# Kernel optimization log

Measured on AMD Instinct MI355X. Metric: run time of the kernel, lower is better.

The kernel has to match this reference:

```python
import jax, jax.numpy as jnp
import numpy as np

D_MODEL = 512
NUM_HEADS = 8
D_K = D_MODEL // NUM_HEADS


def setup_inputs() -> dict:
    key = jax.random.key(0)
    ks = jax.random.split(key, 24)
    inp = {
        "user": jax.random.normal(ks[0], (4, 8192, D_MODEL), jnp.float32),
        "mood": jax.random.normal(ks[1], (3, 8192, D_MODEL), jnp.float32),
        "genre": jax.random.normal(ks[2], (5, 8192, D_MODEL), jnp.float32),
    }
    i = 3
    for p in ["l", "s", "zl", "zs"]:
        inp[p + "_w1"] = jax.random.normal(ks[i], (D_K, D_K), jnp.float32) * 0.1; i += 1
        inp[p + "_b1"] = jax.random.normal(ks[i], (D_K,), jnp.float32) * 0.1; i += 1
        inp[p + "_w2"] = jax.random.normal(ks[i], (D_K,), jnp.float32) * 0.1; i += 1
        inp[p + "_b2"] = jax.random.normal(ks[i], (1,), jnp.float32) * 0.1; i += 1
    inp["lin_w"] = jax.random.normal(ks[i], (D_MODEL, D_MODEL), jnp.float32) * 0.05; i += 1
    inp["lin_b"] = jax.random.normal(ks[i], (D_MODEL,), jnp.float32) * 0.05
    return inp


def _score(x, w1, b1, w2, b2):
    # Linear(d_k,d_k) -> Sigmoid -> Linear(d_k,1); returns [..., 1]
    h = jax.nn.sigmoid(jnp.einsum("...k,jk->...j", x, w1) + b1)
    return (jnp.einsum("...k,k->...", h, w2) + b2)[..., None]


def reference(user, mood, genre,
              l_w1, l_b1, l_w2, l_b2,
              s_w1, s_b1, s_w2, s_b2,
              zl_w1, zl_b1, zl_w2, zl_b2,
              zs_w1, zs_b1, zs_w2, zs_b2,
              lin_w, lin_b):
    scale = 1.0 / np.sqrt(D_K).astype(np.float32)
    Nu, B, D = user.shape
    Nm = mood.shape[0]
    Ng = genre.shape[0]
    # L[u,g] = split_heads(user_u * genre_g) / sqrt(d_k)  -> [Nu, Ng, B, H, d_k]
    L = (user[:, None] * genre[None, :]).reshape(Nu, Ng, B, NUM_HEADS, D_K) * scale
    S = (mood[:, None] * genre[None, :]).reshape(Nm, Ng, B, NUM_HEADS, D_K) * scale
    L_score = _score(L, l_w1, l_b1, l_w2, l_b2)  # [Nu, Ng, B, H, 1]
    S_score = _score(S, s_w1, s_b1, s_w2, s_b2)
    # sum over all key pairs of score * value -> [B, H, d_k]
    L_att = jnp.sum(L_score * L, axis=(0, 1))
    S_att = jnp.sum(S_score * S, axis=(0, 1))
    rl = _score(L_att, zl_w1, zl_b1, zl_w2, zl_b2)  # [B, H, 1]
    rs = _score(S_att, zs_w1, zs_b1, zs_w2, zs_b2)
    r = jax.nn.softmax(jnp.concatenate([rl, rs], axis=-1), axis=-1)
    out = r[..., 0:1] * L_att + r[..., 1:2] * S_att  # [B, H, d_k]
    out = out.reshape(B, NUM_HEADS * D_K)
    return out @ lin_w.T + lin_b
```

## Files before the change

kernel.cpp:

```cpp
#include <hip/hip_runtime.h>
#include <hip/hip_bf16.h>
#include <stdint.h>

#define B_TOK 8192
#define DMODEL 512

typedef __attribute__((ext_vector_type(4))) float f32x4;
typedef __attribute__((ext_vector_type(8))) short bf16x8;
typedef __attribute__((ext_vector_type(4))) short bf16x4;
typedef __attribute__((ext_vector_type(2))) _Float16 f16x2;
typedef __attribute__((ext_vector_type(4))) _Float16 f16x4;
typedef __attribute__((ext_vector_type(8))) _Float16 f16x8;

__device__ __forceinline__ short f2bf(float f) {
    union { float f; uint32_t u; } v; v.f = f;
    uint32_t r = (v.u + 0x7fffu + ((v.u >> 16) & 1u)) >> 16;
    return (short)r;
}

__device__ __forceinline__ f16x2 pkrtz(float a, float b) {
    auto r = __builtin_amdgcn_cvt_pkrtz(a, b);
    union { decltype(r) i; f16x2 o; } u; u.i = r;
    return u.o;
}

__device__ __forceinline__ float sigm2(float x) {
    return __builtin_amdgcn_rcpf(1.0f + __builtin_amdgcn_exp2f(x));
}

#define NL2E (-1.44269504089f)
#define L2E  (1.44269504089f)

struct ScoreW {
    f16x8 w1f[4][2];
    f32x4 b1f[4];
    f16x8 w2f[2];
    f32x4 b2v;
};

template <bool EXPS>
__device__ __forceinline__ void load_scorew(ScoreW& W,
    const float* __restrict__ w1p, const float* __restrict__ b1p,
    const float* __restrict__ w2p, const float* __restrict__ b2p,
    int tl, int g16)
{
    const float scl = EXPS ? NL2E : 1.0f;
    #pragma unroll
    for (int nt = 0; nt < 4; ++nt) {
        const int q  = nt >> 1;
        const int hi = (nt & 1) * 4;
        const int j  = q * 32 + (tl >> 2) * 8 + hi + (tl & 3);
        #pragma unroll
        for (int kk = 0; kk < 2; ++kk) {
            const float* wr = w1p + j * 64 + kk * 32 + g16 * 8;
            f32x4 a0 = *(const f32x4*)wr * scl;
            f32x4 a1 = *(const f32x4*)(wr + 4) * scl;
            f16x2 p0 = pkrtz(a0[0], a0[1]);
            f16x2 p1 = pkrtz(a0[2], a0[3]);
            f16x2 p2 = pkrtz(a1[0], a1[1]);
            f16x2 p3 = pkrtz(a1[2], a1[3]);
            f16x8 f = {p0[0],p0[1],p1[0],p1[1],p2[0],p2[1],p3[0],p3[1]};
            W.w1f[nt][kk] = f;
        }
        W.b1f[nt] = *(const f32x4*)(b1p + q * 32 + g16 * 8 + hi) * scl;
    }
    #pragma unroll
    for (int q = 0; q < 2; ++q) {
        const float* wp = w2p + q * 32 + g16 * 8;
        f32x4 a0 = *(const f32x4*)wp;
        f32x4 a1 = *(const f32x4*)(wp + 4);
        f16x2 p0 = pkrtz(a0[0], a0[1]);
        f16x2 p1 = pkrtz(a0[2], a0[3]);
        f16x2 p2 = pkrtz(a1[0], a1[1]);
        f16x2 p3 = pkrtz(a1[2], a1[3]);
        f16x8 f = {p0[0],p0[1],p1[0],p1[1],p2[0],p2[1],p3[0],p3[1]};
        W.w2f[q] = f;
    }
    const float b2 = b2p[0];
    f32x4 bb = {b2, b2, b2, b2};
    W.b2v = bb;
}

template <bool POLY>
__device__ __forceinline__ f32x4 score16(const ScoreW& W, f16x8 xa0, f16x8 xa1)
{
    f32x4 acc1[4];
    #pragma unroll
    for (int nt = 0; nt < 4; ++nt)
        acc1[nt] = __builtin_amdgcn_mfma_f32_16x16x32_f16(W.w1f[nt][0], xa0, W.b1f[nt], 0, 0, 0);
    #pragma unroll
    for (int nt = 0; nt < 4; ++nt)
        acc1[nt] = __builtin_amdgcn_mfma_f32_16x16x32_f16(W.w1f[nt][1], xa1, acc1[nt], 0, 0, 0);

    f32x4 acc2a = W.b2v;
    f32x4 acc2b = {0.f, 0.f, 0.f, 0.f};
    #pragma unroll
    for (int q = 0; q < 2; ++q) {
        f16x8 sb;
        if constexpr (POLY) {
            const _Float16 c1 = (_Float16)0.25f;
            const _Float16 c2 = (_Float16)(-0.0208333f);
            const _Float16 c3 = (_Float16)(0.00208333f);
            const _Float16 hf = (_Float16)0.5f;
            f16x2 h0 = pkrtz(acc1[2*q][0],   acc1[2*q][1]);
            f16x2 h1 = pkrtz(acc1[2*q][2],   acc1[2*q][3]);
            f16x2 h2 = pkrtz(acc1[2*q+1][0], acc1[2*q+1][1]);
            f16x2 h3 = pkrtz(acc1[2*q+1][2], acc1[2*q+1][3]);
            f16x8 hv = {h0[0],h0[1],h1[0],h1[1],h2[0],h2[1],h3[0],h3[1]};
            f16x8 C1 = {c1,c1,c1,c1,c1,c1,c1,c1};
            f16x8 C2 = {c2,c2,c2,c2,c2,c2,c2,c2};
            f16x8 C3 = {c3,c3,c3,c3,c3,c3,c3,c3};
            f16x8 HF = {hf,hf,hf,hf,hf,hf,hf,hf};
            f16x8 hh = hv * hv;
            f16x8 u  = hh * C3 + C2;
            f16x8 v  = hh * u  + C1;
            sb       = hv * v  + HF;
        } else {
            f16x2 s0 = pkrtz(sigm2(acc1[2*q][0]),   sigm2(acc1[2*q][1]));
            f16x2 s1 = pkrtz(sigm2(acc1[2*q][2]),   sigm2(acc1[2*q][3]));
            f16x2 s2 = pkrtz(sigm2(acc1[2*q+1][0]), sigm2(acc1[2*q+1][1]));
            f16x2 s3 = pkrtz(sigm2(acc1[2*q+1][2]), sigm2(acc1[2*q+1][3]));
            sb = (f16x8){s0[0],s0[1],s1[0],s1[1],s2[0],s2[1],s3[0],s3[1]};
        }
        if (q == 0)
            acc2a = __builtin_amdgcn_mfma_f32_16x16x32_f16(W.w2f[0], sb, acc2a, 0, 0, 0);
        else
            acc2b = __builtin_amdgcn_mfma_f32_16x16x32_f16(W.w2f[1], sb, acc2b, 0, 0, 0);
    }
    return acc2a + acc2b;
}

template <bool WSB>
__global__ __launch_bounds__(256, 3) void fused_att(
    const float* __restrict__ user, const float* __restrict__ mood,
    const float* __restrict__ genre,
    const float* __restrict__ lw1,  const float* __restrict__ lb1,
    const float* __restrict__ lw2,  const float* __restrict__ lb2,
    const float* __restrict__ sw1,  const float* __restrict__ sb1,
    const float* __restrict__ sw2,  const float* __restrict__ sb2,
    const float* __restrict__ zlw1, const float* __restrict__ zlb1,
    const float* __restrict__ zlw2, const float* __restrict__ zlb2,
    const float* __restrict__ zsw1, const float* __restrict__ zsb1,
    const float* __restrict__ zsw2, const float* __restrict__ zsb2,
    float* __restrict__ fout, short* __restrict__ bout)
{
    __shared__ __attribute__((aligned(16))) unsigned char smraw[12 * 32 * 128];
    _Float16* att = (_Float16*)smraw;
    float*    rsc = (float*)(smraw + 20480);

    const int tid  = threadIdx.x;
    const int lane = tid & 63;
    const int wv   = tid >> 6;
    const int tl   = lane & 15;
    const int g16  = lane >> 4;
    const int wg   = blockIdx.x;

    {
        const int k4 = (tid & 15) << 2;
        #pragma unroll
        for (int h = 0; h < 2; ++h) {
            const int r = h * 16 + (tid >> 4);
            const int dst_off = r * 128 + ((k4 * 2) ^ ((r & 7) << 4));
            const size_t src_off = (size_t)wg * 2048 + (size_t)r * 64 + k4;
            #pragma unroll
            for (int a = 0; a < 12; ++a) {
                const float* src; float scl;
                if (a < 4)      { src = user  + (size_t)a       * (B_TOK * DMODEL); scl = 0.125f; }
                else if (a < 9) { src = genre + (size_t)(a - 4) * (B_TOK * DMODEL); scl = 1.0f;  }
                else            { src = mood  + (size_t)(a - 9) * (B_TOK * DMODEL); scl = 0.125f; }
                f32x4 v = *(const f32x4*)(src + src_off) * scl;
                f16x2 lo = pkrtz(v[0], v[1]);
                f16x2 hi = pkrtz(v[2], v[3]);
                f16x4 b = {lo[0], lo[1], hi[0], hi[1]};
                *(f16x4*)(smraw + a * 4096 + dst_off) = b;
            }
        }
    }
    __syncthreads();

    ScoreW W;
    if (wv < 2) load_scorew<false>(W, lw1, lb1, lw2, lb2, tl, g16);
    else        load_scorew<false>(W, sw1, sb1, sw2, sb2, tl, g16);

    int pcount, sbase, pstart;
    if      (wv == 0) { pstart = 0;  pcount = 10; sbase = 0; }
    else if (wv == 1) { pstart = 10; pcount = 10; sbase = 0; }
    else if (wv == 2) { pstart = 0;  pcount = 8;  sbase = 9; }
    else              { pstart = 8;  pcount = 7;  sbase = 9; }

    int aA = sbase + pstart / 5;
    int aB = 4 + pstart % 5;

    f16x8 attA0 = {0,0,0,0,0,0,0,0}, attA1 = {0,0,0,0,0,0,0,0};
    f16x8 attB0 = {0,0,0,0,0,0,0,0}, attB1 = {0,0,0,0,0,0,0,0};

    const unsigned char* lbase = smraw;
    const int rowbA = tl * 128;
    const int rowbB = (16 + tl) * 128;
    const int swz   = (tl & 7) << 4;
    const int ko2   = g16 * 16;
    const int o0 = ko2 ^ swz;
    const int o1 = (ko2 + 64) ^ swz;

    for (int pi = 0; pi < pcount; ++pi) {
        const unsigned char* ub = lbase + aA * 4096;
        const unsigned char* gb = lbase + aB * 4096;
        f16x8 xaA0 = *(const f16x8*)(ub + rowbA + o0) * *(const f16x8*)(gb + rowbA + o0);
        f16x8 xaA1 = *(const f16x8*)(ub + rowbA + o1) * *(const f16x8*)(gb + rowbA + o1);
        f16x8 xaB0 = *(const f16x8*)(ub + rowbB + o0) * *(const f16x8*)(gb + rowbB + o0);
        f16x8 xaB1 = *(const f16x8*)(ub + rowbB + o1) * *(const f16x8*)(gb + rowbB + o1);

        f32x4 scA = score16<true>(W, xaA0, xaA1);
        f32x4 scB = score16<true>(W, xaB0, xaB1);

        _Float16 hA = (_Float16)scA[0];
        _Float16 hB = (_Float16)scB[0];
        f16x8 svA = {hA, hA, hA, hA, hA, hA, hA, hA};
        f16x8 svB = {hB, hB, hB, hB, hB, hB, hB, hB};
        attA0 += svA * xaA0;
        attA1 += svA * xaA1;
        attB0 += svB * xaB0;
        attB1 += svB * xaB1;

        if (++aB == 9) { aB = 4; ++aA; }
    }

    __syncthreads();

    *(f16x8*)(att + (wv * 32 + tl) * 80 + g16 * 8)           = attA0;
    *(f16x8*)(att + (wv * 32 + tl) * 80 + 32 + g16 * 8)      = attA1;
    *(f16x8*)(att + (wv * 32 + 16 + tl) * 80 + g16 * 8)      = attB0;
    *(f16x8*)(att + (wv * 32 + 16 + tl) * 80 + 32 + g16 * 8) = attB1;
    __syncthreads();

    if (wv < 2) {
        ScoreW ZW;
        if (wv == 0) load_scorew<true>(ZW, zlw1, zlb1, zlw2, zlb2, tl, g16);
        else         load_scorew<true>(ZW, zsw1, zsb1, zsw2, zsb2, tl, g16);

        const int b0 = wv * 2, b1i = wv * 2 + 1;
        #pragma unroll
        for (int g = 0; g < 2; ++g) {
            const int r = g * 16 + tl;
            f16x8 za0 = *(const f16x8*)(att + (b0  * 32 + r) * 80 + g16 * 8) +
                        *(const f16x8*)(att + (b1i * 32 + r) * 80 + g16 * 8);
            f16x8 za1 = *(const f16x8*)(att + (b0  * 32 + r) * 80 + 32 + g16 * 8) +
                        *(const f16x8*)(att + (b1i * 32 + r) * 80 + 32 + g16 * 8);
            f32x4 rz = score16<false>(ZW, za0, za1);
            if (g16 == 0) rsc[wv * 32 + r] = rz[0];
        }
    }
    __syncthreads();

    {
        const int k4 = (tid & 15) << 2;
        #pragma unroll
        for (int h = 0; h < 2; ++h) {
            const int r = h * 16 + (tid >> 4);
            f16x4 Lh = *(const f16x4*)(att + (0 * 32 + r) * 80 + k4) +
                       *(const f16x4*)(att + (1 * 32 + r) * 80 + k4);
            f16x4 Sh = *(const f16x4*)(att + (2 * 32 + r) * 80 + k4) +
                       *(const f16x4*)(att + (3 * 32 + r) * 80 + k4);
            const float rl = rsc[r], rs = rsc[32 + r];
            const float r0 = __builtin_amdgcn_rcpf(1.0f + __builtin_amdgcn_exp2f((rs - rl) * L2E));
            float o[4];
            #pragma unroll
            for (int i = 0; i < 4; ++i) {
                const float Lf = (float)Lh[i], Sf = (float)Sh[i];
                o[i] = Sf + (Lf - Sf) * r0;
            }
            const size_t base = (size_t)wg * 2048 + (size_t)r * 64 + k4;
            if constexpr (WSB) {
                bf16x4 b = {f2bf(o[0]), f2bf(o[1]), f2bf(o[2]), f2bf(o[3])};
                *(bf16x4*)(bout + base) = b;
            } else {
                f32x4 mx = {o[0], o[1], o[2], o[3]};
                *(f32x4*)(fout + base) = mx;
            }
        }
    }
}

__global__ __launch_bounds__(256) void conv_w(const float* __restrict__ w,
                                              short* __restrict__ o)
{
    const size_t i = ((size_t)blockIdx.x * 256 + threadIdx.x) * 4;
    f32x4 v = *(const f32x4*)(w + i);
    bf16x4 b;
    b[0] = f2bf(v[0]); b[1] = f2bf(v[1]); b[2] = f2bf(v[2]); b[3] = f2bf(v[3]);
    *(bf16x4*)(o + i) = b;
}

__global__ __launch_bounds__(256, 2) void final_gemm_ws(
    const short* __restrict__ A, const short* __restrict__ Bw,
    const float* __restrict__ bias, float* __restrict__ C)
{
    __shared__ __attribute__((aligned(16))) short lA[64 * 64];
    __shared__ __attribute__((aligned(16))) short lB[128 * 64];

    const int tid  = threadIdx.x;
    const int lane = tid & 63;
    const int wv   = tid >> 6;
    const int tl   = lane & 15;
    const int g16  = lane >> 4;
    const int wr   = wv >> 1;
    const int wc   = wv & 1;
    const int bm   = blockIdx.x & 127;
    const int bn   = blockIdx.x >> 7;
    const int m0   = bm * 64, n0 = bn * 128;

    f32x4 acc[2][4];
    #pragma unroll
    for (int mt = 0; mt < 2; ++mt)
        #pragma unroll
        for (int nt = 0; nt < 4; ++nt) { f32x4 z = {0.f,0.f,0.f,0.f}; acc[mt][nt] = z; }

    bf16x8 ra[2], rb[4];
    auto LD = [&](int ks) {
        #pragma unroll
        for (int i = 0; i < 2; ++i) {
            const int c = tid + i * 256;
            ra[i] = *(const bf16x8*)(A + (size_t)(m0 + (c >> 3)) * 512 + ks * 64 + (c & 7) * 8);
        }
        #pragma unroll
        for (int i = 0; i < 4; ++i) {
            const int c = tid + i * 256;
            rb[i] = *(const bf16x8*)(Bw + (size_t)(n0 + (c >> 3)) * 512 + ks * 64 + (c & 7) * 8);
        }
    };

    LD(0);
    for (int ks = 0; ks < 8; ++ks) {
        __syncthreads();
        #pragma unroll
        for (int i = 0; i < 2; ++i) {
            const int c = tid + i * 256, row = c >> 3;
            *(bf16x8*)(lA + row * 64 + ((c & 7) ^ (row & 7)) * 8) = ra[i];
        }
        #pragma unroll
        for (int i = 0; i < 4; ++i) {
            const int c = tid + i * 256, row = c >> 3;
            *(bf16x8*)(lB + row * 64 + ((c & 7) ^ (row & 7)) * 8) = rb[i];
        }
        __syncthreads();
        if (ks < 7) LD(ks + 1);
        #pragma unroll
        for (int kk = 0; kk < 2; ++kk) {
            bf16x8 af[2], bfr[4];
            #pragma unroll
            for (int mt = 0; mt < 2; ++mt) {
                const int row = wr * 32 + mt * 16 + tl;
                af[mt] = *(const bf16x8*)(lA + row * 64 + ((kk * 4 + g16) ^ (row & 7)) * 8);
            }
            #pragma unroll
            for (int nt = 0; nt < 4; ++nt) {
                const int row = wc * 64 + nt * 16 + tl;
                bfr[nt] = *(const bf16x8*)(lB + row * 64 + ((kk * 4 + g16) ^ (row & 7)) * 8);
            }
            #pragma unroll
            for (int mt = 0; mt < 2; ++mt)
                #pragma unroll
                for (int nt = 0; nt < 4; ++nt)
                    acc[mt][nt] = __builtin_amdgcn_mfma_f32_16x16x32_bf16(af[mt], bfr[nt], acc[mt][nt], 0, 0, 0);
        }
    }

    #pragma unroll
    for (int nt = 0; nt < 4; ++nt) {
        const int n = n0 + wc * 64 + nt * 16 + tl;
        const float bv = bias[n];
        #pragma unroll
        for (int mt = 0; mt < 2; ++mt) {
            #pragma unroll
            for (int r = 0; r < 4; ++r) {
                C[(size_t)(m0 + wr * 32 + mt * 16 + g16 * 4 + r) * 512 + n] = acc[mt][nt][r] + bv;
            }
        }
    }
}

__global__ __launch_bounds__(256, 2) void final_gemm_ip(
    const float* __restrict__ linw, const float* __restrict__ linb, float* io)
{
    const int tid  = threadIdx.x;
    const int lane = tid & 63;
    const int wv   = tid >> 6;
    const int tl   = lane & 15;
    const int g16  = lane >> 4;
    const int row0 = blockIdx.x * 64 + wv * 16;

    f32x4 acc[32];
    #pragma unroll
    for (int nt = 0; nt < 32; ++nt) { f32x4 z = {0.f,0.f,0.f,0.f}; acc[nt] = z; }

    for (int ks = 0; ks < 16; ++ks) {
        const int k0 = ks * 32 + g16 * 8;
        const float* ar = io + (size_t)(row0 + tl) * 512 + k0;
        f32x4 a0 = *(const f32x4*)ar;
        f32x4 a1 = *(const f32x4*)(ar + 4);
        bf16x8 af;
        af[0]=f2bf(a0[0]); af[1]=f2bf(a0[1]); af[2]=f2bf(a0[2]); af[3]=f2bf(a0[3]);
        af[4]=f2bf(a1[0]); af[5]=f2bf(a1[1]); af[6]=f2bf(a1[2]); af[7]=f2bf(a1[3]);
        #pragma unroll
        for (int nt = 0; nt < 32; ++nt) {
            const int n = nt * 16 + tl;
            const float* br = linw + (size_t)n * 512 + k0;
            f32x4 b0 = *(const f32x4*)br;
            f32x4 b1 = *(const f32x4*)(br + 4);
            bf16x8 bv;
            bv[0]=f2bf(b0[0]); bv[1]=f2bf(b0[1]); bv[2]=f2bf(b0[2]); bv[3]=f2bf(b0[3]);
            bv[4]=f2bf(b1[0]); bv[5]=f2bf(b1[1]); bv[6]=f2bf(b1[2]); bv[7]=f2bf(b1[3]);
            acc[nt] = __builtin_amdgcn_mfma_f32_16x16x32_bf16(af, bv, acc[nt], 0, 0, 0);
        }
    }

    #pragma unroll
    for (int nt = 0; nt < 32; ++nt) {
        const int n = nt * 16 + tl;
        const float lb = linb[n];
        #pragma unroll
        for (int r = 0; r < 4; ++r)
            io[(size_t)(row0 + g16 * 4 + r) * 512 + n] = acc[nt][r] + lb;
    }
}

extern "C" void kernel_launch(void* const* d_in, const int* in_sizes, int n_in,
                              void* d_out, int out_size, void* d_ws, size_t ws_size,
                              hipStream_t stream)
{
    const float* user = (const float*)d_in[0];
    const float* mood = (const float*)d_in[1];
    const float* genre= (const float*)d_in[2];
    const float* lw1  = (const float*)d_in[3];
    const float* lb1  = (const float*)d_in[4];
    const float* lw2  = (const float*)d_in[5];
    const float* lb2  = (const float*)d_in[6];
    const float* sw1  = (const float*)d_in[7];
    const float* sb1  = (const float*)d_in[8];
    const float* sw2  = (const float*)d_in[9];
    const float* sb2  = (const float*)d_in[10];
    const float* zlw1 = (const float*)d_in[11];
    const float* zlb1 = (const float*)d_in[12];
    const float* zlw2 = (const float*)d_in[13];
    const float* zlb2 = (const float*)d_in[14];
    const float* zsw1 = (const float*)d_in[15];
    const float* zsb1 = (const float*)d_in[16];
    const float* zsw2 = (const float*)d_in[17];
    const float* zsb2 = (const float*)d_in[18];
    const float* linw = (const float*)d_in[19];
    const float* linb = (const float*)d_in[20];
    float* out = (float*)d_out;

    const size_t WNEED = (size_t)512 * 512 * 2 + (size_t)B_TOK * 512 * 2;
    if (ws_size >= WNEED) {
        short* wb   = (short*)d_ws;
        short* mixb = wb + 512 * 512;
        conv_w<<<256, 256, 0, stream>>>(linw, wb);
        fused_att<true><<<B_TOK / 4, 256, 0, stream>>>(
            user, mood, genre,
            lw1, lb1, lw2, lb2, sw1, sb1, sw2, sb2,
            zlw1, zlb1, zlw2, zlb2, zsw1, zsb1, zsw2, zsb2,
            nullptr, mixb);
        final_gemm_ws<<<512, 256, 0, stream>>>(mixb, wb, linb, out);
    } else {
        fused_att<false><<<B_TOK / 4, 256, 0, stream>>>(
            user, mood, genre,
            lw1, lb1, lw2, lb2, sw1, sb1, sw2, sb2,
            zlw1, zlb1, zlw2, zlb2, zsw1, zsb1, zsw2, zsb2,
            out, nullptr);
        final_gemm_ip<<<B_TOK / 64, 256, 0, stream>>>(linw, linb, out);
    }
}
```

Measured before the change: 75.82 us.

## Load inputs directly into registers and split attention work by row instead of pair

```diff
diff --git a/kernel.cpp b/kernel.cpp
--- a/kernel.cpp
+++ b/kernel.cpp
@@ -31,6 +31,16 @@
 #define NL2E (-1.44269504089f)
 #define L2E  (1.44269504089f)
 
+__device__ __forceinline__ f16x8 ldh(const float* __restrict__ p, float scl) {
+    f32x4 a0 = *(const f32x4*)p * scl;
+    f32x4 a1 = *(const f32x4*)(p + 4) * scl;
+    f16x2 p0 = pkrtz(a0[0], a0[1]);
+    f16x2 p1 = pkrtz(a0[2], a0[3]);
+    f16x2 p2 = pkrtz(a1[0], a1[1]);
+    f16x2 p3 = pkrtz(a1[2], a1[3]);
+    return (f16x8){p0[0],p0[1],p1[0],p1[1],p2[0],p2[1],p3[0],p3[1]};
+}
+
 struct ScoreW {
     f16x8 w1f[4][2];
     f32x4 b1f[4];
@@ -51,31 +61,13 @@
         const int hi = (nt & 1) * 4;
         const int j  = q * 32 + (tl >> 2) * 8 + hi + (tl & 3);
         #pragma unroll
-        for (int kk = 0; kk < 2; ++kk) {
-            const float* wr = w1p + j * 64 + kk * 32 + g16 * 8;
-            f32x4 a0 = *(const f32x4*)wr * scl;
-            f32x4 a1 = *(const f32x4*)(wr + 4) * scl;
-            f16x2 p0 = pkrtz(a0[0], a0[1]);
-            f16x2 p1 = pkrtz(a0[2], a0[3]);
-            f16x2 p2 = pkrtz(a1[0], a1[1]);
-            f16x2 p3 = pkrtz(a1[2], a1[3]);
-            f16x8 f = {p0[0],p0[1],p1[0],p1[1],p2[0],p2[1],p3[0],p3[1]};
-            W.w1f[nt][kk] = f;
-        }
+        for (int kk = 0; kk < 2; ++kk)
+            W.w1f[nt][kk] = ldh(w1p + j * 64 + kk * 32 + g16 * 8, scl);
         W.b1f[nt] = *(const f32x4*)(b1p + q * 32 + g16 * 8 + hi) * scl;
     }
     #pragma unroll
-    for (int q = 0; q < 2; ++q) {
-        const float* wp = w2p + q * 32 + g16 * 8;
-        f32x4 a0 = *(const f32x4*)wp;
-        f32x4 a1 = *(const f32x4*)(wp + 4);
-        f16x2 p0 = pkrtz(a0[0], a0[1]);
-        f16x2 p1 = pkrtz(a0[2], a0[3]);
-        f16x2 p2 = pkrtz(a1[0], a1[1]);
-        f16x2 p3 = pkrtz(a1[2], a1[3]);
-        f16x8 f = {p0[0],p0[1],p1[0],p1[1],p2[0],p2[1],p3[0],p3[1]};
-        W.w2f[q] = f;
-    }
+    for (int q = 0; q < 2; ++q)
+        W.w2f[q] = ldh(w2p + q * 32 + g16 * 8, 1.0f);
     const float b2 = b2p[0];
     f32x4 bb = {b2, b2, b2, b2};
     W.b2v = bb;
@@ -131,7 +123,7 @@
 }
 
 template <bool WSB>
-__global__ __launch_bounds__(256, 3) void fused_att(
+__global__ __launch_bounds__(256, 2) void fused_att(
     const float* __restrict__ user, const float* __restrict__ mood,
     const float* __restrict__ genre,
     const float* __restrict__ lw1,  const float* __restrict__ lb1,
@@ -144,9 +136,9 @@
     const float* __restrict__ zsw2, const float* __restrict__ zsb2,
     float* __restrict__ fout, short* __restrict__ bout)
 {
-    __shared__ __attribute__((aligned(16))) unsigned char smraw[12 * 32 * 128];
-    _Float16* att = (_Float16*)smraw;
-    float*    rsc = (float*)(smraw + 20480);
+    __shared__ __attribute__((aligned(16))) _Float16 attL[32][80];
+    __shared__ __attribute__((aligned(16))) _Float16 attS[32][80];
+    __shared__ float rls[2][32];
 
     const int tid  = threadIdx.x;
     const int lane = tid & 63;
@@ -155,128 +147,106 @@
     const int g16  = lane >> 4;
     const int wg   = blockIdx.x;
 
+    const int  rbase  = (wv & 1) * 16;
+    const bool isL    = (wv < 2);
+    const size_t rowoff = ((size_t)wg * 32 + rbase + tl) * 64 + g16 * 8;
+
+    ScoreW W;
+    if (isL) load_scorew<false>(W, lw1, lb1, lw2, lb2, tl, g16);
+    else     load_scorew<false>(W, sw1, sb1, sw2, sb2, tl, g16);
+
+    f16x8 att0 = {0,0,0,0,0,0,0,0};
+    f16x8 att1 = {0,0,0,0,0,0,0,0};
+
+    if (isL) {
+        f16x8 uf[4][2], gf[5][2];
+        #pragma unroll
+        for (int a = 0; a < 4; ++a) {
+            const float* p = user + (size_t)a * (B_TOK * DMODEL) + rowoff;
+            uf[a][0] = ldh(p, 0.125f);
+            uf[a][1] = ldh(p + 32, 0.125f);
+        }
+        #pragma unroll
+        for (int a = 0; a < 5; ++a) {
+            const float* p = genre + (size_t)a * (B_TOK * DMODEL) + rowoff;
+            gf[a][0] = ldh(p, 1.0f);
+            gf[a][1] = ldh(p + 32, 1.0f);
+        }
+        #pragma unroll
+        for (int pi = 0; pi < 20; ++pi) {
+            const int aA = pi / 5, aB = pi % 5;
+            f16x8 xa0 = uf[aA][0] * gf[aB][0];
+            f16x8 xa1 = uf[aA][1] * gf[aB][1];
+            f32x4 sc = score16<true>(W, xa0, xa1);
+            _Float16 hs = (_Float16)sc[0];
+            f16x8 sv = {hs,hs,hs,hs,hs,hs,hs,hs};
+            att0 += sv * xa0;
+            att1 += sv * xa1;
+        }
+    } else {
+        f16x8 mf[3][2], gf[5][2];
+        #pragma unroll
+        for (int a = 0; a < 3; ++a) {
+            const float* p = mood + (size_t)a * (B_TOK * DMODEL) + rowoff;
+            mf[a][0] = ldh(p, 0.125f);
+            mf[a][1] = ldh(p + 32, 0.125f);
+        }
+        #pragma unroll
+        for (int a = 0; a < 5; ++a) {
+            const float* p = genre + (size_t)a * (B_TOK * DMODEL) + rowoff;
+            gf[a][0] = ldh(p, 1.0f);
+            gf[a][1] = ldh(p + 32, 1.0f);
+        }
+        #pragma unroll
+        for (int pi = 0; pi < 15; ++pi) {
+            const int aA = pi / 5, aB = pi % 5;
+            f16x8 xa0 = mf[aA][0] * gf[aB][0];
+            f16x8 xa1 = mf[aA][1] * gf[aB][1];
+            f32x4 sc = score16<true>(W, xa0, xa1);
+            _Float16 hs = (_Float16)sc[0];
+            f16x8 sv = {hs,hs,hs,hs,hs,hs,hs,hs};
+            att0 += sv * xa0;
+            att1 += sv * xa1;
+        }
+    }
+
+    ScoreW ZW;
+    if (isL) load_scorew<true>(ZW, zlw1, zlb1, zlw2, zlb2, tl, g16);
+    else     load_scorew<true>(ZW, zsw1, zsb1, zsw2, zsb2, tl, g16);
+    f32x4 rz = score16<false>(ZW, att0, att1);
+
     {
-        const int k4 = (tid & 15) << 2;
-        #pragma unroll
-        for (int h = 0; h < 2; ++h) {
-            const int r = h * 16 + (tid >> 4);
-            const int dst_off = r * 128 + ((k4 * 2) ^ ((r & 7) << 4));
-            const size_t src_off = (size_t)wg * 2048 + (size_t)r * 64 + k4;
+        _Float16* ap = isL ? &attL[rbase + tl][0] : &attS[rbase + tl][0];
+        *(f16x8*)(ap + g16 * 8)      = att0;
+        *(f16x8*)(ap + 32 + g16 * 8) = att1;
+        if (g16 == 0) rls[isL ? 0 : 1][rbase + tl] = rz[0];
+    }
+    __syncthreads();
+
+    {
+        const int r  = tid >> 3;
+        const int k8 = (tid & 7) * 8;
+        f16x8 Lh = *(const f16x8*)&attL[r][k8];
+        f16x8 Sh = *(const f16x8*)&attS[r][k8];
+        const float rl = rls[0][r], rs = rls[1][r];
+        const float r0 = __builtin_amdgcn_rcpf(1.0f + __builtin_amdgcn_exp2f((rs - rl) * L2E));
+        float o[8];
+        #pragma unroll
+        for (int i = 0; i < 8; ++i) {
+            const float Lf = (float)Lh[i], Sf = (float)Sh[i];
+            o[i] = Sf + (Lf - Sf) * r0;
+        }
+        const size_t base = (size_t)wg * 2048 + (size_t)r * 64 + k8;
+        if constexpr (WSB) {
+            bf16x8 b;
             #pragma unroll
-            for (int a = 0; a < 12; ++a) {
-                const float* src; float scl;
-                if (a < 4)      { src = user  + (size_t)a       * (B_TOK * DMODEL); scl = 0.125f; }
-                else if (a < 9) { src = genre + (size_t)(a - 4) * (B_TOK * DMODEL); scl = 1.0f;  }
-                else            { src = mood  + (size_t)(a - 9) * (B_TOK * DMODEL); scl = 0.125f; }
-                f32x4 v = *(const f32x4*)(src + src_off) * scl;
-                f16x2 lo = pkrtz(v[0], v[1]);
-                f16x2 hi = pkrtz(v[2], v[3]);
-                f16x4 b = {lo[0], lo[1], hi[0], hi[1]};
-                *(f16x4*)(smraw + a * 4096 + dst_off) = b;
-            }
-        }
-    }
-    __syncthreads();
-
-    ScoreW W;
-    if (wv < 2) load_scorew<false>(W, lw1, lb1, lw2, lb2, tl, g16);
-    else        load_scorew<false>(W, sw1, sb1, sw2, sb2, tl, g16);
-
-    int pcount, sbase, pstart;
-    if      (wv == 0) { pstart = 0;  pcount = 10; sbase = 0; }
-    else if (wv == 1) { pstart = 10; pcount = 10; sbase = 0; }
-    else if (wv == 2) { pstart = 0;  pcount = 8;  sbase = 9; }
-    else              { pstart = 8;  pcount = 7;  sbase = 9; }
-
-    int aA = sbase + pstart / 5;
-    int aB = 4 + pstart % 5;
-
-    f16x8 attA0 = {0,0,0,0,0,0,0,0}, attA1 = {0,0,0,0,0,0,0,0};
-    f16x8 attB0 = {0,0,0,0,0,0,0,0}, attB1 = {0,0,0,0,0,0,0,0};
-
-    const unsigned char* lbase = smraw;
-    const int rowbA = tl * 128;
-    const int rowbB = (16 + tl) * 128;
-    const int swz   = (tl & 7) << 4;
-    const int ko2   = g16 * 16;
-    const int o0 = ko2 ^ swz;
-    const int o1 = (ko2 + 64) ^ swz;
-
-    for (int pi = 0; pi < pcount; ++pi) {
-        const unsigned char* ub = lbase + aA * 4096;
-        const unsigned char* gb = lbase + aB * 4096;
-        f16x8 xaA0 = *(const f16x8*)(ub + rowbA + o0) * *(const f16x8*)(gb + rowbA + o0);
-        f16x8 xaA1 = *(const f16x8*)(ub + rowbA + o1) * *(const f16x8*)(gb + rowbA + o1);
-        f16x8 xaB0 = *(const f16x8*)(ub + rowbB + o0) * *(const f16x8*)(gb + rowbB + o0);
-        f16x8 xaB1 = *(const f16x8*)(ub + rowbB + o1) * *(const f16x8*)(gb + rowbB + o1);
-
-        f32x4 scA = score16<true>(W, xaA0, xaA1);
-        f32x4 scB = score16<true>(W, xaB0, xaB1);
-
-        _Float16 hA = (_Float16)scA[0];
-        _Float16 hB = (_Float16)scB[0];
-        f16x8 svA = {hA, hA, hA, hA, hA, hA, hA, hA};
-        f16x8 svB = {hB, hB, hB, hB, hB, hB, hB, hB};
-        attA0 += svA * xaA0;
-        attA1 += svA * xaA1;
-        attB0 += svB * xaB0;
-        attB1 += svB * xaB1;
-
-        if (++aB == 9) { aB = 4; ++aA; }
-    }
-
-    __syncthreads();
-
-    *(f16x8*)(att + (wv * 32 + tl) * 80 + g16 * 8)           = attA0;
-    *(f16x8*)(att + (wv * 32 + tl) * 80 + 32 + g16 * 8)      = attA1;
-    *(f16x8*)(att + (wv * 32 + 16 + tl) * 80 + g16 * 8)      = attB0;
-    *(f16x8*)(att + (wv * 32 + 16 + tl) * 80 + 32 + g16 * 8) = attB1;
-    __syncthreads();
-
-    if (wv < 2) {
-        ScoreW ZW;
-        if (wv == 0) load_scorew<true>(ZW, zlw1, zlb1, zlw2, zlb2, tl, g16);
-        else         load_scorew<true>(ZW, zsw1, zsb1, zsw2, zsb2, tl, g16);
-
-        const int b0 = wv * 2, b1i = wv * 2 + 1;
-        #pragma unroll
-        for (int g = 0; g < 2; ++g) {
-            const int r = g * 16 + tl;
-            f16x8 za0 = *(const f16x8*)(att + (b0  * 32 + r) * 80 + g16 * 8) +
-                        *(const f16x8*)(att + (b1i * 32 + r) * 80 + g16 * 8);
-            f16x8 za1 = *(const f16x8*)(att + (b0  * 32 + r) * 80 + 32 + g16 * 8) +
-                        *(const f16x8*)(att + (b1i * 32 + r) * 80 + 32 + g16 * 8);
-            f32x4 rz = score16<false>(ZW, za0, za1);
-            if (g16 == 0) rsc[wv * 32 + r] = rz[0];
-        }
-    }
-    __syncthreads();
-
-    {
-        const int k4 = (tid & 15) << 2;
-        #pragma unroll
-        for (int h = 0; h < 2; ++h) {
-            const int r = h * 16 + (tid >> 4);
-            f16x4 Lh = *(const f16x4*)(att + (0 * 32 + r) * 80 + k4) +
-                       *(const f16x4*)(att + (1 * 32 + r) * 80 + k4);
-            f16x4 Sh = *(const f16x4*)(att + (2 * 32 + r) * 80 + k4) +
-                       *(const f16x4*)(att + (3 * 32 + r) * 80 + k4);
-            const float rl = rsc[r], rs = rsc[32 + r];
-            const float r0 = __builtin_amdgcn_rcpf(1.0f + __builtin_amdgcn_exp2f((rs - rl) * L2E));
-            float o[4];
-            #pragma unroll
-            for (int i = 0; i < 4; ++i) {
-                const float Lf = (float)Lh[i], Sf = (float)Sh[i];
-                o[i] = Sf + (Lf - Sf) * r0;
-            }
-            const size_t base = (size_t)wg * 2048 + (size_t)r * 64 + k4;
-            if constexpr (WSB) {
-                bf16x4 b = {f2bf(o[0]), f2bf(o[1]), f2bf(o[2]), f2bf(o[3])};
-                *(bf16x4*)(bout + base) = b;
-            } else {
-                f32x4 mx = {o[0], o[1], o[2], o[3]};
-                *(f32x4*)(fout + base) = mx;
-            }
+            for (int i = 0; i < 8; ++i) b[i] = f2bf(o[i]);
+            *(bf16x8*)(bout + base) = b;
+        } else {
+            f32x4 m0 = {o[0], o[1], o[2], o[3]};
+            f32x4 m1 = {o[4], o[5], o[6], o[7]};
+            *(f32x4*)(fout + base)     = m0;
+            *(f32x4*)(fout + base + 4) = m1;
         }
     }
 }
```

Result: slower. 87.58 us (+15.5%).

## Pre-pack score weights to fp16 fragments, prefetch LDS operands, raise MFMA priority

Applied to the files above, without the earlier changes.

```diff
diff --git a/kernel.cpp b/kernel.cpp
--- a/kernel.cpp
+++ b/kernel.cpp
@@ -31,6 +31,16 @@
 #define NL2E (-1.44269504089f)
 #define L2E  (1.44269504089f)
 
+__device__ __forceinline__ f16x8 ldh(const float* __restrict__ p, float scl) {
+    f32x4 a0 = *(const f32x4*)p * scl;
+    f32x4 a1 = *(const f32x4*)(p + 4) * scl;
+    f16x2 p0 = pkrtz(a0[0], a0[1]);
+    f16x2 p1 = pkrtz(a0[2], a0[3]);
+    f16x2 p2 = pkrtz(a1[0], a1[1]);
+    f16x2 p3 = pkrtz(a1[2], a1[3]);
+    return (f16x8){p0[0],p0[1],p1[0],p1[1],p2[0],p2[1],p3[0],p3[1]};
+}
+
 struct ScoreW {
     f16x8 w1f[4][2];
     f32x4 b1f[4];
@@ -51,46 +61,49 @@
         const int hi = (nt & 1) * 4;
         const int j  = q * 32 + (tl >> 2) * 8 + hi + (tl & 3);
         #pragma unroll
-        for (int kk = 0; kk < 2; ++kk) {
-            const float* wr = w1p + j * 64 + kk * 32 + g16 * 8;
-            f32x4 a0 = *(const f32x4*)wr * scl;
-            f32x4 a1 = *(const f32x4*)(wr + 4) * scl;
-            f16x2 p0 = pkrtz(a0[0], a0[1]);
-            f16x2 p1 = pkrtz(a0[2], a0[3]);
-            f16x2 p2 = pkrtz(a1[0], a1[1]);
-            f16x2 p3 = pkrtz(a1[2], a1[3]);
-            f16x8 f = {p0[0],p0[1],p1[0],p1[1],p2[0],p2[1],p3[0],p3[1]};
-            W.w1f[nt][kk] = f;
-        }
+        for (int kk = 0; kk < 2; ++kk)
+            W.w1f[nt][kk] = ldh(w1p + j * 64 + kk * 32 + g16 * 8, scl);
         W.b1f[nt] = *(const f32x4*)(b1p + q * 32 + g16 * 8 + hi) * scl;
     }
     #pragma unroll
-    for (int q = 0; q < 2; ++q) {
-        const float* wp = w2p + q * 32 + g16 * 8;
-        f32x4 a0 = *(const f32x4*)wp;
-        f32x4 a1 = *(const f32x4*)(wp + 4);
-        f16x2 p0 = pkrtz(a0[0], a0[1]);
-        f16x2 p1 = pkrtz(a0[2], a0[3]);
-        f16x2 p2 = pkrtz(a1[0], a1[1]);
-        f16x2 p3 = pkrtz(a1[2], a1[3]);
-        f16x8 f = {p0[0],p0[1],p1[0],p1[1],p2[0],p2[1],p3[0],p3[1]};
-        W.w2f[q] = f;
-    }
+    for (int q = 0; q < 2; ++q)
+        W.w2f[q] = ldh(w2p + q * 32 + g16 * 8, 1.0f);
     const float b2 = b2p[0];
     f32x4 bb = {b2, b2, b2, b2};
     W.b2v = bb;
 }
 
+__device__ __forceinline__ void load_scorew_pre(ScoreW& W,
+    const _Float16* __restrict__ swf, const float* __restrict__ b1fp,
+    const float* __restrict__ b2fp, int branch, int lane)
+{
+    #pragma unroll
+    for (int nt = 0; nt < 4; ++nt)
+        #pragma unroll
+        for (int kk = 0; kk < 2; ++kk)
+            W.w1f[nt][kk] = *(const f16x8*)(swf + ((size_t)(branch * 10 + nt * 2 + kk) * 64 + lane) * 8);
+    W.w2f[0] = *(const f16x8*)(swf + ((size_t)(branch * 10 + 8) * 64 + lane) * 8);
+    W.w2f[1] = *(const f16x8*)(swf + ((size_t)(branch * 10 + 9) * 64 + lane) * 8);
+    #pragma unroll
+    for (int nt = 0; nt < 4; ++nt)
+        W.b1f[nt] = *(const f32x4*)(b1fp + ((size_t)(branch * 4 + nt) * 64 + lane) * 4);
+    const float b2 = b2fp[branch];
+    f32x4 bb = {b2, b2, b2, b2};
+    W.b2v = bb;
+}
+
 template <bool POLY>
 __device__ __forceinline__ f32x4 score16(const ScoreW& W, f16x8 xa0, f16x8 xa1)
 {
     f32x4 acc1[4];
+    __builtin_amdgcn_s_setprio(1);
     #pragma unroll
     for (int nt = 0; nt < 4; ++nt)
         acc1[nt] = __builtin_amdgcn_mfma_f32_16x16x32_f16(W.w1f[nt][0], xa0, W.b1f[nt], 0, 0, 0);
     #pragma unroll
     for (int nt = 0; nt < 4; ++nt)
         acc1[nt] = __builtin_amdgcn_mfma_f32_16x16x32_f16(W.w1f[nt][1], xa1, acc1[nt], 0, 0, 0);
+    __builtin_amdgcn_s_setprio(0);
 
     f32x4 acc2a = W.b2v;
     f32x4 acc2b = {0.f, 0.f, 0.f, 0.f};
@@ -100,7 +113,7 @@
         if constexpr (POLY) {
             const _Float16 c1 = (_Float16)0.25f;
             const _Float16 c2 = (_Float16)(-0.0208333f);
-            const _Float16 c3 = (_Float16)(0.00208333f);
+            const _Float16 c3 = (_Float16)0.00208333f;
             const _Float16 hf = (_Float16)0.5f;
             f16x2 h0 = pkrtz(acc1[2*q][0],   acc1[2*q][1]);
             f16x2 h1 = pkrtz(acc1[2*q][2],   acc1[2*q][3]);
@@ -122,10 +135,12 @@
             f16x2 s3 = pkrtz(sigm2(acc1[2*q+1][2]), sigm2(acc1[2*q+1][3]));
             sb = (f16x8){s0[0],s0[1],s1[0],s1[1],s2[0],s2[1],s3[0],s3[1]};
         }
+        __builtin_amdgcn_s_setprio(1);
         if (q == 0)
             acc2a = __builtin_amdgcn_mfma_f32_16x16x32_f16(W.w2f[0], sb, acc2a, 0, 0, 0);
         else
             acc2b = __builtin_amdgcn_mfma_f32_16x16x32_f16(W.w2f[1], sb, acc2b, 0, 0, 0);
+        __builtin_amdgcn_s_setprio(0);
     }
     return acc2a + acc2b;
 }
@@ -142,6 +157,8 @@
     const float* __restrict__ zlw2, const float* __restrict__ zlb2,
     const float* __restrict__ zsw1, const float* __restrict__ zsb1,
     const float* __restrict__ zsw2, const float* __restrict__ zsb2,
+    const _Float16* __restrict__ swf, const float* __restrict__ b1fp,
+    const float* __restrict__ b2fp,
     float* __restrict__ fout, short* __restrict__ bout)
 {
     __shared__ __attribute__((aligned(16))) unsigned char smraw[12 * 32 * 128];
@@ -179,8 +196,12 @@
     __syncthreads();
 
     ScoreW W;
-    if (wv < 2) load_scorew<false>(W, lw1, lb1, lw2, lb2, tl, g16);
-    else        load_scorew<false>(W, sw1, sb1, sw2, sb2, tl, g16);
+    if constexpr (WSB) {
+        load_scorew_pre(W, swf, b1fp, b2fp, (wv < 2) ? 0 : 1, lane);
+    } else {
+        if (wv < 2) load_scorew<false>(W, lw1, lb1, lw2, lb2, tl, g16);
+        else        load_scorew<false>(W, sw1, sb1, sw2, sb2, tl, g16);
+    }
 
     int pcount, sbase, pstart;
     if      (wv == 0) { pstart = 0;  pcount = 10; sbase = 0; }
@@ -202,27 +223,45 @@
     const int o0 = ko2 ^ swz;
     const int o1 = (ko2 + 64) ^ swz;
 
+    auto rd = [&](int arr, int rowb, int off) -> f16x8 {
+        return *(const f16x8*)(lbase + arr * 4096 + rowb + off);
+    };
+
+    f16x8 uA0 = rd(aA, rowbA, o0), uA1 = rd(aA, rowbA, o1);
+    f16x8 uB0 = rd(aA, rowbB, o0), uB1 = rd(aA, rowbB, o1);
+    f16x8 gA0 = rd(aB, rowbA, o0), gA1 = rd(aB, rowbA, o1);
+    f16x8 gB0 = rd(aB, rowbB, o0), gB1 = rd(aB, rowbB, o1);
+
     for (int pi = 0; pi < pcount; ++pi) {
-        const unsigned char* ub = lbase + aA * 4096;
-        const unsigned char* gb = lbase + aB * 4096;
-        f16x8 xaA0 = *(const f16x8*)(ub + rowbA + o0) * *(const f16x8*)(gb + rowbA + o0);
-        f16x8 xaA1 = *(const f16x8*)(ub + rowbA + o1) * *(const f16x8*)(gb + rowbA + o1);
-        f16x8 xaB0 = *(const f16x8*)(ub + rowbB + o0) * *(const f16x8*)(gb + rowbB + o0);
-        f16x8 xaB1 = *(const f16x8*)(ub + rowbB + o1) * *(const f16x8*)(gb + rowbB + o1);
+        f16x8 xaA0 = uA0 * gA0, xaA1 = uA1 * gA1;
+        f16x8 xaB0 = uB0 * gB0, xaB1 = uB1 * gB1;
+
+        f16x8 ngA0 = gA0, ngA1 = gA1, ngB0 = gB0, ngB1 = gB1;
+        if (pi + 1 < pcount) {
+            int nB = aB + 1;
+            if (nB == 9) {
+                nB = 4; ++aA;
+                uA0 = rd(aA, rowbA, o0); uA1 = rd(aA, rowbA, o1);
+                uB0 = rd(aA, rowbB, o0); uB1 = rd(aA, rowbB, o1);
+            }
+            aB = nB;
+            ngA0 = rd(aB, rowbA, o0); ngA1 = rd(aB, rowbA, o1);
+            ngB0 = rd(aB, rowbB, o0); ngB1 = rd(aB, rowbB, o1);
+        }
 
         f32x4 scA = score16<true>(W, xaA0, xaA1);
         f32x4 scB = score16<true>(W, xaB0, xaB1);
 
         _Float16 hA = (_Float16)scA[0];
         _Float16 hB = (_Float16)scB[0];
-        f16x8 svA = {hA, hA, hA, hA, hA, hA, hA, hA};
-        f16x8 svB = {hB, hB, hB, hB, hB, hB, hB, hB};
+        f16x8 svA = {hA,hA,hA,hA,hA,hA,hA,hA};
+        f16x8 svB = {hB,hB,hB,hB,hB,hB,hB,hB};
         attA0 += svA * xaA0;
         attA1 += svA * xaA1;
         attB0 += svB * xaB0;
         attB1 += svB * xaB1;
 
-        if (++aB == 9) { aB = 4; ++aA; }
+        gA0 = ngA0; gA1 = ngA1; gB0 = ngB0; gB1 = ngB1;
     }
 
     __syncthreads();
@@ -235,9 +274,12 @@
 
     if (wv < 2) {
         ScoreW ZW;
-        if (wv == 0) load_scorew<true>(ZW, zlw1, zlb1, zlw2, zlb2, tl, g16);
-        else         load_scorew<true>(ZW, zsw1, zsb1, zsw2, zsb2, tl, g16);
-
+        if constexpr (WSB) {
+            load_scorew_pre(ZW, swf, b1fp, b2fp, (wv == 0) ? 2 : 3, lane);
+        } else {
+            if (wv == 0) load_scorew<true>(ZW, zlw1, zlb1, zlw2, zlb2, tl, g16);
+            else         load_scorew<true>(ZW, zsw1, zsb1, zsw2, zsb2, tl, g16);
+        }
         const int b0 = wv * 2, b1i = wv * 2 + 1;
         #pragma unroll
         for (int g = 0; g < 2; ++g) {
@@ -289,6 +331,56 @@
     bf16x4 b;
     b[0] = f2bf(v[0]); b[1] = f2bf(v[1]); b[2] = f2bf(v[2]); b[3] = f2bf(v[3]);
     *(bf16x4*)(o + i) = b;
+}
+
+__global__ __launch_bounds__(256) void conv_sw(
+    const float* __restrict__ lw1,  const float* __restrict__ lb1,
+    const float* __restrict__ lw2,  const float* __restrict__ lb2,
+    const float* __restrict__ sw1,  const float* __restrict__ sb1,
+    const float* __restrict__ sw2,  const float* __restrict__ sb2,
+    const float* __restrict__ zlw1, const float* __restrict__ zlb1,
+    const float* __restrict__ zlw2, const float* __restrict__ zlb2,
+    const float* __restrict__ zsw1, const float* __restrict__ zsb1,
+    const float* __restrict__ zsw2, const float* __restrict__ zsb2,
+    _Float16* __restrict__ swf, float* __restrict__ b1f, float* __restrict__ b2f)
+{
+    const int blk = blockIdx.x, tid = threadIdx.x;
+    if (blk < 80) {
+        const int idx = blk * 256 + tid;
+        const int e = idx & 7;
+        int t = idx >> 3;
+        const int lane = t & 63; t >>= 6;
+        const int f = t % 10;
+        const int branch = t / 10;
+        const int tl = lane & 15, g16 = lane >> 4;
+        const float* w1p = (branch == 0) ? lw1 : (branch == 1) ? sw1 : (branch == 2) ? zlw1 : zsw1;
+        const float* w2p = (branch == 0) ? lw2 : (branch == 1) ? sw2 : (branch == 2) ? zlw2 : zsw2;
+        float val;
+        if (f < 8) {
+            const int nt = f >> 1, kk = f & 1;
+            const int q = nt >> 1, hi = (nt & 1) * 4;
+            const int j = q * 32 + (tl >> 2) * 8 + hi + (tl & 3);
+            val = w1p[j * 64 + kk * 32 + g16 * 8 + e];
+            if (branch >= 2) val *= NL2E;
+        } else {
+            const int q = f - 8;
+            val = w2p[q * 32 + g16 * 8 + e];
+        }
+        swf[idx] = (_Float16)val;
+    } else {
+        const int idx = (blk - 80) * 256 + tid;
+        const int branch = idx >> 8, nt = (idx >> 6) & 3, lane = idx & 63;
+        const int q = nt >> 1, hi = (nt & 1) * 4, g16 = lane >> 4;
+        const float* b1p = (branch == 0) ? lb1 : (branch == 1) ? sb1 : (branch == 2) ? zlb1 : zsb1;
+        const float scl = (branch >= 2) ? NL2E : 1.0f;
+        #pragma unroll
+        for (int c = 0; c < 4; ++c)
+            b1f[idx * 4 + c] = b1p[q * 32 + g16 * 8 + hi + c] * scl;
+        if (blk == 80 && tid < 4) {
+            const float* b2p = (tid == 0) ? lb2 : (tid == 1) ? sb2 : (tid == 2) ? zlb2 : zsb2;
+            b2f[tid] = b2p[0];
+        }
+    }
 }
 
 __global__ __launch_bounds__(256, 2) void final_gemm_ws(
@@ -451,23 +543,34 @@
     const float* linb = (const float*)d_in[20];
     float* out = (float*)d_out;
 
-    const size_t WNEED = (size_t)512 * 512 * 2 + (size_t)B_TOK * 512 * 2;
+    const size_t SWF_ELTS = (size_t)4 * 10 * 64 * 8;
+    const size_t B1F_ELTS = (size_t)4 * 4 * 64 * 4;
+    const size_t WNEED = (size_t)512 * 512 * 2 + (size_t)B_TOK * 512 * 2
+                       + SWF_ELTS * 2 + (B1F_ELTS + 4) * 4;
+
     if (ws_size >= WNEED) {
-        short* wb   = (short*)d_ws;
-        short* mixb = wb + 512 * 512;
+        short*     wb   = (short*)d_ws;
+        short*     mixb = wb + 512 * 512;
+        _Float16*  swf  = (_Float16*)(mixb + (size_t)B_TOK * 512);
+        float*     b1f  = (float*)(swf + SWF_ELTS);
+        float*     b2f  = b1f + B1F_ELTS;
+
         conv_w<<<256, 256, 0, stream>>>(linw, wb);
+        conv_sw<<<84, 256, 0, stream>>>(lw1, lb1, lw2, lb2, sw1, sb1, sw2, sb2,
+                                        zlw1, zlb1, zlw2, zlb2, zsw1, zsb1, zsw2, zsb2,
+                                        swf, b1f, b2f);
         fused_att<true><<<B_TOK / 4, 256, 0, stream>>>(
             user, mood, genre,
             lw1, lb1, lw2, lb2, sw1, sb1, sw2, sb2,
             zlw1, zlb1, zlw2, zlb2, zsw1, zsb1, zsw2, zsb2,
-            nullptr, mixb);
+            swf, b1f, b2f, nullptr, mixb);
         final_gemm_ws<<<512, 256, 0, stream>>>(mixb, wb, linb, out);
     } else {
         fused_att<false><<<B_TOK / 4, 256, 0, stream>>>(
             user, mood, genre,
             lw1, lb1, lw2, lb2, sw1, sb1, sw2, sb2,
             zlw1, zlb1, zlw2, zlb2, zsw1, zsb1, zsw2, zsb2,
-            out, nullptr);
+            nullptr, nullptr, nullptr, out, nullptr);
         final_gemm_ip<<<B_TOK / 64, 256, 0, stream>>>(linw, linb, out);
     }
 }
```

Measured after the change: 71.84 us, median of 2. -5.2%, faster.
